# Performance work log

Measured on AMD Instinct MI355X. Metric: run time of the kernel, lower is better.

Reference implementation:

```python
import jax, jax.numpy as jnp
import numpy as np

T, B, D = 1024, 64, 512  # time, batch, d_model (input feat == d_model)

def setup_inputs() -> dict:
    key = jax.random.key(0)
    k1, k2, k3 = jax.random.split(key, 3)
    inputs = jax.random.normal(k1, (T, B, D), dtype=jnp.float32)
    # scale weights to avoid gate saturation over long sequences
    Wi = jax.random.normal(k2, (D, 4 * D), dtype=jnp.float32) * 0.05
    Wh = jax.random.normal(k3, (D, 4 * D), dtype=jnp.float32) * 0.05
    b = jnp.zeros((4 * D,), dtype=jnp.float32)
    c0 = jnp.zeros((B, D), dtype=jnp.float32)
    h0 = jnp.zeros((B, D), dtype=jnp.float32)
    return {"inputs": inputs, "c0": c0, "h0": h0, "Wi": Wi, "Wh": Wh, "b": b}

def reference(inputs, c0, h0, Wi, Wh, b):
    # Faithful flax OptimizedLSTMCell scanned over time (time-major inputs).
    def step(carry, x):
        c, h = carry
        z = x @ Wi + h @ Wh + b            # [B, 4D]
        i, f, g, o = jnp.split(z, 4, axis=-1)  # flax gate order i, f, g, o
        new_c = jax.nn.sigmoid(f) * c + jax.nn.sigmoid(i) * jnp.tanh(g)
        new_h = jax.nn.sigmoid(o) * jnp.tanh(new_c)
        return (new_c, new_h), new_h
    (cT, hT), ys = jax.lax.scan(step, (c0, h0), inputs)
    return ys, cT, hT
```

## Files before the change

### kernel.cpp

```cpp
#include <hip/hip_runtime.h>
#include <hip/hip_bf16.h>
#include <stdint.h>

#define T_STEPS 1024
#define NBLK    64
#define NTHR    512
#define TPB     16

typedef __attribute__((ext_vector_type(8))) short short8;
typedef __attribute__((ext_vector_type(4))) float float4v;
typedef unsigned short ushort_t;
typedef unsigned long long ull;
typedef unsigned int u32;

__device__ __forceinline__ ushort_t f2bf(float f) {
    __hip_bfloat16 h = __float2bfloat16(f);
    return __builtin_bit_cast(ushort_t, h);
}

__global__ void lstm_setup(const float* __restrict__ Wi,
                           const float* __restrict__ Wh,
                           const float* __restrict__ h0,
                           ushort_t* __restrict__ WiT,
                           ushort_t* __restrict__ WhT,
                           ushort_t* __restrict__ ring,
                           u32* __restrict__ flag) {
    size_t i = (size_t)blockIdx.x * NTHR + threadIdx.x;
    if (i < 1048576) {
        size_t c = i >> 9, k = i & 511;
        WiT[i] = f2bf(Wi[k * 2048 + c]);
    } else if (i < 2097152) {
        size_t j = i - 1048576;
        size_t c = j >> 9, k = j & 511;
        WhT[j] = f2bf(Wh[k * 2048 + c]);
    } else if (i < 2129920) {
        size_t j = i - 2097152;
        size_t ch = j >> 9, row = (j >> 3) & 63, c = j & 7;
        ring[32768 + j] = f2bf(h0[row * 512 + ch * 8 + c]);
    } else if (i < 2130432) {
        flag[i - 2129920] = 0u;
    }
}

__global__ __launch_bounds__(NTHR, 2) void lstm_pregemm(
    const float* __restrict__ X,
    const float* __restrict__ bias,
    const ushort_t* __restrict__ WiT,
    float* __restrict__ zx,
    int t0)
{
    const int blk  = blockIdx.x & 63;
    const int tch  = blockIdx.x >> 6;
    const int tid  = threadIdx.x;
    const int lane = tid & 63;
    const int w    = tid >> 6;
    const int l15  = lane & 15;
    const int quad = lane >> 4;
    const int nt   = w & 1;
    const int mi   = w >> 1;

    __shared__ alignas(16) char smem[65536];

    const int col = (l15 >> 2) * 512 + blk * 8 + nt * 4 + (l15 & 3);
    short8 wib[16];
    {
        const short8* wp = (const short8*)(WiT + (size_t)col * 512);
#pragma unroll
        for (int kk = 0; kk < 16; kk++) wib[kk] = wp[kk * 4 + quad];
    }
    const float bval = bias[col];
    const int cg = (nt * 4 + (l15 & 3)) * 4 + (l15 >> 2);

    const int xrow = tid & 63;
    const int xseg = tid >> 6;

    for (int tt = 0; tt < TPB; tt++) {
        const int tc = tch * TPB + tt;
        const int t  = t0 + tc;
        {
            const float* xb = X + (size_t)t * 32768 + xrow * 512 + xseg * 64;
#pragma unroll
            for (int jj = 0; jj < 8; jj++) {
                float4v a = *(const float4v*)(xb + jj * 8);
                float4v b = *(const float4v*)(xb + jj * 8 + 4);
                short8 p;
                p[0] = (short)f2bf(a.x); p[1] = (short)f2bf(a.y);
                p[2] = (short)f2bf(a.z); p[3] = (short)f2bf(a.w);
                p[4] = (short)f2bf(b.x); p[5] = (short)f2bf(b.y);
                p[6] = (short)f2bf(b.z); p[7] = (short)f2bf(b.w);
                *(short8*)(smem + (xseg * 8 + jj) * 1024 + xrow * 16) = p;
            }
        }
        __syncthreads();

        float4v acc = {bval, bval, bval, bval};
#pragma unroll
        for (int kk = 0; kk < 16; kk++) {
            short8 a = *(const short8*)(smem + (kk * 4 + quad) * 1024 +
                                        (mi * 16 + l15) * 16);
            acc = __builtin_amdgcn_mfma_f32_16x16x32_bf16(a, wib[kk], acc, 0, 0, 0);
        }

        {
            float* zrow = zx + (size_t)(tc * 64 + blk) * 2048;
#pragma unroll
            for (int r = 0; r < 4; r++)
                zrow[(mi * 16 + quad * 4 + r) * 32 + cg] = acc[r];
        }
        __syncthreads();
    }
}

__global__ __launch_bounds__(NTHR, 2) void lstm_persist_zx(
    const float* __restrict__ c_src,
    const ushort_t* __restrict__ WhT,
    const float* __restrict__ zx,
    ushort_t* __restrict__ ring,
    u32* __restrict__ flag,
    float* __restrict__ out,
    int t0, int nsteps,
    float* __restrict__ csave)
{
    const int blk  = blockIdx.x;
    const int tid  = threadIdx.x;
    const int lane = tid & 63;
    const int w    = tid >> 6;
    const int l15  = lane & 15;
    const int quad = lane >> 4;
    const int nt   = w & 1;
    const int mi   = w >> 1;

    __shared__ alignas(16) char smem[65536];

    const int col = (l15 >> 2) * 512 + blk * 8 + nt * 4 + (l15 & 3);
    short8 whb[16];
    {
        const short8* hp = (const short8*)(WhT + (size_t)col * 512);
#pragma unroll
        for (int kk = 0; kk < 16; kk++) whb[kk] = hp[kk * 4 + quad];
    }

    const int crow = mi * 16 + quad * 4 + (l15 >> 2);
    const int ccol = nt * 4 + (l15 & 3);
    float c_reg = c_src[crow * 512 + blk * 8 + ccol];

    float*    ztile_w = (float*)(smem + w * 1088);
    ushort_t* hout_w  = (ushort_t*)(smem + 8704 + w * 128);

    const float* zbase = zx + (size_t)blk * 2048 + (size_t)crow * 32 + ccol * 4;

    for (int tc = 0; tc < nsteps; tc++) {
        const int t = t0 + tc;

        float4v zx4 = *(const float4v*)(zbase + (size_t)tc * 131072);

        if (t > 0 && w == 0) {
            const unsigned tgt = (unsigned)t;
            for (;;) {
                unsigned v = __hip_atomic_load(&flag[lane * 8], __ATOMIC_RELAXED,
                                               __HIP_MEMORY_SCOPE_AGENT);
                if (__ballot(v >= tgt) == ~0ull) break;
                __builtin_amdgcn_s_sleep(1);
            }
        }
        __syncthreads();

        {
            const ushort_t* rslot = ring + (size_t)((t + 1) & 1) * 32768;
#pragma unroll
            for (int j = 0; j < 8; j++) {
                int f = w * 8 + j;
                const u32 __attribute__((address_space(1)))* gp =
                    (const u32 __attribute__((address_space(1)))*)(rslot + f * 512 + lane * 8);
                u32 __attribute__((address_space(3)))* lp =
                    (u32 __attribute__((address_space(3)))*)(smem + f * 1024);
                __builtin_amdgcn_global_load_lds(gp, lp, 16, 0, 17);
            }
        }
        __syncthreads();

        float4v acc = {0.f, 0.f, 0.f, 0.f};
#pragma unroll
        for (int kk = 0; kk < 16; kk++) {
            short8 a = *(const short8*)(smem + (kk * 4 + quad) * 1024 +
                                        (mi * 16 + l15) * 16);
            acc = __builtin_amdgcn_mfma_f32_16x16x32_bf16(a, whb[kk], acc, 0, 0, 0);
        }
        __syncthreads();

#pragma unroll
        for (int r = 0; r < 4; r++)
            ztile_w[(quad * 4 + r) * 17 + l15] = acc[r];
        float zi = ztile_w[(quad * 4 + (l15 >> 2)) * 17 + 0  + (l15 & 3)] + zx4.x;
        float zf = ztile_w[(quad * 4 + (l15 >> 2)) * 17 + 4  + (l15 & 3)] + zx4.y;
        float zg = ztile_w[(quad * 4 + (l15 >> 2)) * 17 + 8  + (l15 & 3)] + zx4.z;
        float zo = ztile_w[(quad * 4 + (l15 >> 2)) * 17 + 12 + (l15 & 3)] + zx4.w;
        float si = 1.f / (1.f + __expf(-zi));
        float sf = 1.f / (1.f + __expf(-zf));
        float tg = tanhf(zg);
        float so = 1.f / (1.f + __expf(-zo));
        float nc = sf * c_reg + si * tg;
        float nh = so * tanhf(nc);
        c_reg = nc;
        hout_w[(quad * 4 + (l15 >> 2)) * 4 + (l15 & 3)] = f2bf(nh);

        if (lane < 16) {
            ull v = *(const ull*)(hout_w + lane * 4);
            ull* dst = (ull*)(ring + (size_t)(t & 1) * 32768 +
                              blk * 512 + (mi * 16 + lane) * 8 + nt * 4);
            __hip_atomic_store(dst, v, __ATOMIC_RELAXED, __HIP_MEMORY_SCOPE_AGENT);
        }
        __syncthreads();
        if (tid == 0)
            __hip_atomic_store(&flag[blk * 8], (unsigned)(t + 1),
                               __ATOMIC_RELAXED, __HIP_MEMORY_SCOPE_AGENT);

        out[(size_t)t * 32768 + crow * 512 + blk * 8 + ccol] = nh;
        if (t == T_STEPS - 1) {
            out[33554432u + crow * 512 + blk * 8 + ccol] = nc;
            out[33554432u + 32768u + crow * 512 + blk * 8 + ccol] = nh;
        }
    }

    csave[crow * 512 + blk * 8 + ccol] = c_reg;
}

__global__ __launch_bounds__(NTHR, 2) void lstm_persist(
    const float* __restrict__ X,
    const float* __restrict__ c0,
    const float* __restrict__ bias,
    const ushort_t* __restrict__ WiT,
    const ushort_t* __restrict__ WhT,
    ushort_t* __restrict__ ring,
    u32* __restrict__ flag,
    float* __restrict__ out)
{
    const int blk  = blockIdx.x;
    const int tid  = threadIdx.x;
    const int lane = tid & 63;
    const int w    = tid >> 6;
    const int l15  = lane & 15;
    const int quad = lane >> 4;
    const int nt   = w & 1;
    const int mi   = w >> 1;

    __shared__ alignas(16) char smem[65536];

    const int col = (l15 >> 2) * 512 + blk * 8 + nt * 4 + (l15 & 3);
    short8 wib[16], whb[16];
    {
        const short8* wp = (const short8*)(WiT + (size_t)col * 512);
        const short8* hp = (const short8*)(WhT + (size_t)col * 512);
#pragma unroll
        for (int kk = 0; kk < 16; kk++) {
            wib[kk] = wp[kk * 4 + quad];
            whb[kk] = hp[kk * 4 + quad];
        }
    }
    const float bval = bias[col];

    const int crow = mi * 16 + quad * 4 + (l15 >> 2);
    const int ccol = nt * 4 + (l15 & 3);
    float c_reg = c0[crow * 512 + blk * 8 + ccol];

    const int xrow = tid & 63;
    const int xseg = tid >> 6;

    float*    ztile_w = (float*)(smem + w * 1088);
    ushort_t* hout_w  = (ushort_t*)(smem + 8704 + w * 128);

    for (int t = 0; t < T_STEPS; t++) {
        {
            const float* xb = X + (size_t)t * 32768 + xrow * 512 + xseg * 64;
#pragma unroll
            for (int jj = 0; jj < 8; jj++) {
                float4v a = *(const float4v*)(xb + jj * 8);
                float4v b = *(const float4v*)(xb + jj * 8 + 4);
                short8 p;
                p[0] = (short)f2bf(a.x); p[1] = (short)f2bf(a.y);
                p[2] = (short)f2bf(a.z); p[3] = (short)f2bf(a.w);
                p[4] = (short)f2bf(b.x); p[5] = (short)f2bf(b.y);
                p[6] = (short)f2bf(b.z); p[7] = (short)f2bf(b.w);
                *(short8*)(smem + (xseg * 8 + jj) * 1024 + xrow * 16) = p;
            }
        }
        __syncthreads();

        float4v acc = {bval, bval, bval, bval};
#pragma unroll
        for (int kk = 0; kk < 16; kk++) {
            short8 a = *(const short8*)(smem + (kk * 4 + quad) * 1024 +
                                        (mi * 16 + l15) * 16);
            acc = __builtin_amdgcn_mfma_f32_16x16x32_bf16(a, wib[kk], acc, 0, 0, 0);
        }

        if (t > 0 && w == 0) {
            const unsigned tgt = (unsigned)t;
            for (;;) {
                unsigned v = __hip_atomic_load(&flag[lane * 8], __ATOMIC_RELAXED,
                                               __HIP_MEMORY_SCOPE_AGENT);
                if (__ballot(v >= tgt) == ~0ull) break;
                __builtin_amdgcn_s_sleep(1);
            }
        }
        __syncthreads();

        {
            const ushort_t* rslot = ring + (size_t)((t + 1) & 1) * 32768;
#pragma unroll
            for (int j = 0; j < 8; j++) {
                int f = w * 8 + j;
                const u32 __attribute__((address_space(1)))* gp =
                    (const u32 __attribute__((address_space(1)))*)(rslot + f * 512 + lane * 8);
                u32 __attribute__((address_space(3)))* lp =
                    (u32 __attribute__((address_space(3)))*)(smem + f * 1024);
                __builtin_amdgcn_global_load_lds(gp, lp, 16, 0, 17);
            }
        }
        __syncthreads();

#pragma unroll
        for (int kk = 0; kk < 16; kk++) {
            short8 a = *(const short8*)(smem + (kk * 4 + quad) * 1024 +
                                        (mi * 16 + l15) * 16);
            acc = __builtin_amdgcn_mfma_f32_16x16x32_bf16(a, whb[kk], acc, 0, 0, 0);
        }
        __syncthreads();

#pragma unroll
        for (int r = 0; r < 4; r++)
            ztile_w[(quad * 4 + r) * 17 + l15] = acc[r];
        float zi = ztile_w[(quad * 4 + (l15 >> 2)) * 17 + 0  + (l15 & 3)];
        float zf = ztile_w[(quad * 4 + (l15 >> 2)) * 17 + 4  + (l15 & 3)];
        float zg = ztile_w[(quad * 4 + (l15 >> 2)) * 17 + 8  + (l15 & 3)];
        float zo = ztile_w[(quad * 4 + (l15 >> 2)) * 17 + 12 + (l15 & 3)];
        float si = 1.f / (1.f + __expf(-zi));
        float sf = 1.f / (1.f + __expf(-zf));
        float tg = tanhf(zg);
        float so = 1.f / (1.f + __expf(-zo));
        float nc = sf * c_reg + si * tg;
        float nh = so * tanhf(nc);
        c_reg = nc;
        hout_w[(quad * 4 + (l15 >> 2)) * 4 + (l15 & 3)] = f2bf(nh);

        if (lane < 16) {
            ull v = *(const ull*)(hout_w + lane * 4);
            ull* dst = (ull*)(ring + (size_t)(t & 1) * 32768 +
                              blk * 512 + (mi * 16 + lane) * 8 + nt * 4);
            __hip_atomic_store(dst, v, __ATOMIC_RELAXED, __HIP_MEMORY_SCOPE_AGENT);
        }
        __syncthreads();
        if (tid == 0)
            __hip_atomic_store(&flag[blk * 8], (unsigned)(t + 1),
                               __ATOMIC_RELAXED, __HIP_MEMORY_SCOPE_AGENT);

        out[(size_t)t * 32768 + crow * 512 + blk * 8 + ccol] = nh;
        if (t == T_STEPS - 1) {
            out[33554432u + crow * 512 + blk * 8 + ccol] = nc;
            out[33554432u + 32768u + crow * 512 + blk * 8 + ccol] = nh;
        }
    }
}

extern "C" void kernel_launch(void* const* d_in, const int* in_sizes, int n_in,
                              void* d_out, int out_size, void* d_ws, size_t ws_size,
                              hipStream_t stream) {
    const float* X    = (const float*)d_in[0];
    const float* c0   = (const float*)d_in[1];
    const float* h0   = (const float*)d_in[2];
    const float* Wi   = (const float*)d_in[3];
    const float* Wh   = (const float*)d_in[4];
    const float* bias = (const float*)d_in[5];

    char* ws = (char*)d_ws;
    ushort_t* WiT   = (ushort_t*)ws;
    ushort_t* WhT   = (ushort_t*)(ws + 2097152);
    ushort_t* ring  = (ushort_t*)(ws + 4194304);
    u32*      flag  = (u32*)(ws + 4325376);
    float*    csave = (float*)(ws + 4327424);

    lstm_setup<<<4161, NTHR, 0, stream>>>(Wi, Wh, h0, WiT, WhT, ring, flag);

    const size_t ZXOFF = 4458496ull;
    int TC = 0;
    const int cands[6] = {1024, 512, 256, 128, 64, 32};
    for (int i = 0; i < 6; i++) {
        if (ZXOFF + (size_t)cands[i] * 524288ull <= ws_size) { TC = cands[i]; break; }
    }

    if (TC) {
        float* zx = (float*)(ws + ZXOFF);
        const int nch = T_STEPS / TC;
        for (int c = 0; c < nch; c++) {
            const int t0 = c * TC;
            lstm_pregemm<<<(TC / TPB) * 64, NTHR, 0, stream>>>(X, bias, WiT, zx, t0);
            lstm_persist_zx<<<NBLK, NTHR, 0, stream>>>(
                c ? (const float*)csave : c0, WhT, zx, ring, flag,
                (float*)d_out, t0, TC, csave);
        }
    } else {
        lstm_persist<<<NBLK, NTHR, 0, stream>>>(X, c0, bias, WiT, WhT, ring, flag,
                                                (float*)d_out);
    }
}
```

Baseline: 4.056 ms.

## Widen pre-GEMM blocks to 256 columns to reuse converted X tiles

The input-projection pre-GEMM now has each block compute 256 output columns (8 blocks per time chunk instead of 64). Each wave holds two column tiles of Wi in registers and covers all four 16-row tiles, so every bf16 X tile staged in shared memory feeds 8 MFMAs instead of 1. This removes repeated global loads and fp32→bf16 conversion of X across 64 blocks. The cost is more registers per thread (two 16-entry weight arrays plus 8 accumulators) and 8x fewer blocks, which lowers parallelism in the pre-GEMM.

After: 3.314 ms. -18.3%, faster.

```diff
diff --git a/kernel.cpp b/kernel.cpp
--- a/kernel.cpp
+++ b/kernel.cpp
@@ -49,27 +49,31 @@
     float* __restrict__ zx,
     int t0)
 {
-    const int blk  = blockIdx.x & 63;
-    const int tch  = blockIdx.x >> 6;
+    const int ng   = blockIdx.x & 7;
+    const int tch  = blockIdx.x >> 3;
     const int tid  = threadIdx.x;
     const int lane = tid & 63;
     const int w    = tid >> 6;
     const int l15  = lane & 15;
     const int quad = lane >> 4;
-    const int nt   = w & 1;
-    const int mi   = w >> 1;
+    const int g    = w >> 1;
+    const int half = w & 1;
 
     __shared__ alignas(16) char smem[65536];
 
-    const int col = (l15 >> 2) * 512 + blk * 8 + nt * 4 + (l15 & 3);
-    short8 wib[16];
-    {
-        const short8* wp = (const short8*)(WiT + (size_t)col * 512);
-#pragma unroll
-        for (int kk = 0; kk < 16; kk++) wib[kk] = wp[kk * 4 + quad];
-    }
-    const float bval = bias[col];
-    const int cg = (nt * 4 + (l15 & 3)) * 4 + (l15 >> 2);
+    short8 wib[2][16];
+    float  bv[2];
+    int    blkc[2];
+#pragma unroll
+    for (int ct = 0; ct < 2; ct++) {
+        const int c = g * 512 + ng * 64 + half * 32 + ct * 16 + l15;
+        const short8* wp = (const short8*)(WiT + (size_t)c * 512);
+#pragma unroll
+        for (int kk = 0; kk < 16; kk++) wib[ct][kk] = wp[kk * 4 + quad];
+        bv[ct]   = bias[c];
+        blkc[ct] = ng * 8 + half * 4 + ct * 2 + (l15 >> 3);
+    }
+    const int cc = l15 & 7;
 
     const int xrow = tid & 63;
     const int xseg = tid >> 6;
@@ -93,19 +97,32 @@
         }
         __syncthreads();
 
-        float4v acc = {bval, bval, bval, bval};
+        float4v acc[2][4];
+#pragma unroll
+        for (int ct = 0; ct < 2; ct++)
+#pragma unroll
+            for (int rt = 0; rt < 4; rt++)
+                acc[ct][rt] = (float4v){bv[ct], bv[ct], bv[ct], bv[ct]};
+
 #pragma unroll
         for (int kk = 0; kk < 16; kk++) {
-            short8 a = *(const short8*)(smem + (kk * 4 + quad) * 1024 +
-                                        (mi * 16 + l15) * 16);
-            acc = __builtin_amdgcn_mfma_f32_16x16x32_bf16(a, wib[kk], acc, 0, 0, 0);
-        }
-
-        {
-            float* zrow = zx + (size_t)(tc * 64 + blk) * 2048;
-#pragma unroll
-            for (int r = 0; r < 4; r++)
-                zrow[(mi * 16 + quad * 4 + r) * 32 + cg] = acc[r];
+#pragma unroll
+            for (int rt = 0; rt < 4; rt++) {
+                short8 a = *(const short8*)(smem + (kk * 4 + quad) * 1024 +
+                                            (rt * 16 + l15) * 16);
+                acc[0][rt] = __builtin_amdgcn_mfma_f32_16x16x32_bf16(a, wib[0][kk], acc[0][rt], 0, 0, 0);
+                acc[1][rt] = __builtin_amdgcn_mfma_f32_16x16x32_bf16(a, wib[1][kk], acc[1][rt], 0, 0, 0);
+            }
+        }
+
+#pragma unroll
+        for (int ct = 0; ct < 2; ct++) {
+            float* zb = zx + ((size_t)(tc * 64 + blkc[ct]) * 64) * 32 + cc * 4 + g;
+#pragma unroll
+            for (int rt = 0; rt < 4; rt++)
+#pragma unroll
+                for (int r = 0; r < 4; r++)
+                    zb[(size_t)(rt * 16 + quad * 4 + r) * 32] = acc[ct][rt][r];
         }
         __syncthreads();
     }
@@ -393,7 +410,7 @@
         const int nch = T_STEPS / TC;
         for (int c = 0; c < nch; c++) {
             const int t0 = c * TC;
-            lstm_pregemm<<<(TC / TPB) * 64, NTHR, 0, stream>>>(X, bias, WiT, zx, t0);
+            lstm_pregemm<<<(TC / TPB) * 8, NTHR, 0, stream>>>(X, bias, WiT, zx, t0);
             lstm_persist_zx<<<NBLK, NTHR, 0, stream>>>(
                 c ? (const float*)csave : c0, WhT, zx, ring, flag,
                 (float*)d_out, t0, TC, csave);
```
